# Performance work log

Measured on AMD Instinct MI355X. Metric: run time of the kernel, lower is better.

The kernel has to match this reference:

```python
import jax, jax.numpy as jnp
import numpy as np

B, T, L = 64, 2048, 200
H = KV = 256          # hidden_size == key_value_size (asserted in original)
E = 256               # embed_size
V = 33                # vocab_size
MLP_H = 512
EPS = 1e-12           # F.normalize eps


def _p(k, shape):
    return jax.random.normal(k, shape, dtype=jnp.float32) * 0.05


def setup_inputs() -> dict:
    key = jax.random.key(0)
    ks = jax.random.split(key, 20)
    inp = {
        "key":   jax.random.normal(ks[0], (B, T, KV), dtype=jnp.float32),
        "value": jax.random.normal(ks[1], (B, T, KV), dtype=jnp.float32),
        "labels": jax.random.randint(ks[2], (L, B), 0, V).astype(jnp.int32),
        "final_seq_lens": jax.random.randint(ks[3], (B,), 1, T + 1).astype(jnp.int32),
        # embedding table: vocab_size + 1 rows (SOS/padding extra row)
        "emb": _p(ks[4], (V + 1, E)),
        # LSTMCell 0: input = embed + KV
        "w_ih0": _p(ks[5], (4 * H, E + KV)),
        "w_hh0": _p(ks[6], (4 * H, H)),
        "b_ih0": _p(ks[7], (4 * H,)),
        "b_hh0": _p(ks[8], (4 * H,)),
        # LSTMCells 1..2 (n_layers-1 = 2), stacked
        "w_ih_rest": _p(ks[9], (2, 4 * H, H)),
        "w_hh_rest": _p(ks[10], (2, 4 * H, H)),
        "b_ih_rest": _p(ks[11], (2, 4 * H)),
        "b_hh_rest": _p(ks[12], (2, 4 * H)),
        # MLP head: (H + KV) -> MLP_H -> V
        "fc1_w": _p(ks[13], (MLP_H, H + KV)),
        "fc1_b": _p(ks[14], (MLP_H,)),
        "fc2_w": _p(ks[15], (V, MLP_H)),
        "fc2_b": _p(ks[16], (V,)),
    }
    return inp


def _lstm_cell(x, h, c, w_ih, w_hh, b_ih, b_hh):
    # torch.nn.LSTMCell: gates in order i, f, g, o
    g = x @ w_ih.T + b_ih + h @ w_hh.T + b_hh
    i, f, gg, o = jnp.split(g, 4, axis=-1)
    c2 = jax.nn.sigmoid(f) * c + jax.nn.sigmoid(i) * jnp.tanh(gg)
    h2 = jax.nn.sigmoid(o) * jnp.tanh(c2)
    return h2, c2


def reference(key, value, labels, final_seq_lens, emb,
              w_ih0, w_hh0, b_ih0, b_hh0,
              w_ih_rest, w_hh_rest, b_ih_rest, b_hh_rest,
              fc1_w, fc1_b, fc2_w, fc2_b):
    # key mask over encoder time steps: [B, T]
    mask = (jnp.arange(T)[None, :] < final_seq_lens[:, None]).astype(key.dtype)

    labels_emb = emb[labels]                 # [L, B, E] (teacher forcing inputs)

    h0 = jnp.zeros((3, B, H), dtype=key.dtype)
    c0 = jnp.zeros((3, B, H), dtype=key.dtype)
    ctx0 = jnp.zeros((B, KV), dtype=key.dtype)

    def step(carry, x_t):
        h, c, ctx = carry
        rnn_in = jnp.concatenate([x_t, ctx], axis=-1)        # [B, E+KV]
        nh0, nc0 = _lstm_cell(rnn_in, h[0], c[0], w_ih0, w_hh0, b_ih0, b_hh0)
        hs, cs = [nh0], [nc0]
        prev = nh0
        for li in range(2):
            nhi, nci = _lstm_cell(prev, h[li + 1], c[li + 1],
                                  w_ih_rest[li], w_hh_rest[li],
                                  b_ih_rest[li], b_hh_rest[li])
            hs.append(nhi); cs.append(nci)
            prev = nhi
        rnn_out = prev                                       # [B, H]
        # attention: softmax over T, then mask, then L1 renormalize
        energy = jnp.einsum('btd,bd->bt', key, rnn_out)      # [B, T]
        att = jax.nn.softmax(energy, axis=1) * mask
        att = att / jnp.maximum(att.sum(axis=1, keepdims=True), EPS)
        new_ctx = jnp.einsum('bt,btd->bd', att, value)       # [B, KV]
        z = jnp.concatenate([rnn_out, new_ctx], axis=-1)     # [B, H+KV]
        y_t = jnp.maximum(z @ fc1_w.T + fc1_b, 0.0) @ fc2_w.T + fc2_b  # [B, V]
        return (jnp.stack(hs), jnp.stack(cs), new_ctx), y_t

    _, ys = jax.lax.scan(step, (h0, c0, ctx0), labels_emb)   # ys: [L, B, V]
    y_hat = jnp.transpose(ys, (1, 0, 2))                     # [B, L, V]
    return y_hat
```

## Files before the change

### kernel.cpp

```cpp
#include <hip/hip_runtime.h>
#include <hip/hip_bf16.h>

namespace {
constexpr int B  = 64;
constexpr int T  = 2048;
constexpr int L  = 200;
constexpr int H  = 256;
constexpr int KV = 256;
constexpr int E  = 256;
constexpr int V  = 33;
constexpr int MH = 512;
constexpr int G  = 4 * H;
constexpr int HB = H * B;
constexpr int KVB = KV * B;
constexpr int CS = 50;

constexpr long OFF_H   = 0;
constexpr long OFF_C   = OFF_H  + 2L * 3 * HB;
constexpr long OFF_CTX = OFF_C  + 3L * HB;
constexpr long OFF_Z   = OFF_CTX + 2L * KV * B;
constexpr long OFF_M   = OFF_Z  + 2L * B;
constexpr long OFF_E   = OFF_M  + B;
constexpr long OFF_HID = OFF_E  + (long)B * T;
constexpr long OFF_XE  = OFF_HID + (long)MH * B;
constexpr long FLOATS_OLD = OFF_XE + (long)L * E * B;
constexpr long FLOATBYTES = FLOATS_OLD * 4;
constexpr long KVELEMS = (long)B * T * KV;
constexpr long NEED_BF = FLOATBYTES + 2 * KVELEMS * 2;

constexpr long NOFF      = NEED_BF / 4;
constexpr long NOFF_H01  = NOFF;
constexpr long NOFF_C    = NOFF_H01 + 4L * HB;
constexpr long NOFF_H2   = NOFF_C   + 3L * HB;
constexpr long NOFF_CTXA = NOFF_H2  + (long)(L + 1) * HB;
constexpr long NOFF_ZA   = NOFF_CTXA + (long)(L + 1) * KVB;
constexpr long NOFF_HIDC = NOFF_ZA  + (long)(L + 1) * B;
constexpr long FLOATS_NEW = NOFF_HIDC + (long)CS * MH * B;
constexpr long NEED_NEW   = FLOATS_NEW * 4;
}

__device__ __forceinline__ float sigm(float x) { return 1.f / (1.f + __expf(-x)); }
__device__ __forceinline__ float tanh_f(float x) {
  float xc = fminf(fmaxf(x, -15.f), 15.f);
  float e2 = __expf(2.f * xc);
  return (e2 - 1.f) / (e2 + 1.f);
}
__device__ __forceinline__ ushort f2bf(float x) {
  unsigned u = __float_as_uint(x);
  unsigned r = (u + 0x7fffu + ((u >> 16) & 1u)) >> 16;
  return (ushort)r;
}
__device__ __forceinline__ float bf2f(unsigned v) { return __uint_as_float(v << 16); }

__device__ __forceinline__ float gload(const float* p) {
  return __hip_atomic_load(p, __ATOMIC_RELAXED, __HIP_MEMORY_SCOPE_AGENT);
}
__device__ __forceinline__ void gstore(float* p, float v) {
  __hip_atomic_store(p, v, __ATOMIC_RELAXED, __HIP_MEMORY_SCOPE_AGENT);
}

__device__ __forceinline__ void atomicMaxFloat(float* p, float v) {
  int old = __float_as_int(*p);
  while (__int_as_float(old) < v) {
    int assumed = old;
    old = atomicCAS((int*)p, assumed, __float_as_int(v));
    if (old == assumed) break;
  }
}

__device__ __forceinline__ void gbar(unsigned* bar, unsigned gen) {
  __syncthreads();
  if (threadIdx.x == 0) {
    asm volatile("s_waitcnt vmcnt(0)" ::: "memory");
    const unsigned g = blockIdx.x >> 5;
    unsigned prev = __hip_atomic_fetch_add(bar + g * 64, 1u,
                                           __ATOMIC_RELAXED, __HIP_MEMORY_SCOPE_AGENT);
    if (prev == gen * 32u - 1u)
      __hip_atomic_store(bar + 512 + g * 64, gen,
                         __ATOMIC_RELAXED, __HIP_MEMORY_SCOPE_AGENT);
    unsigned spins = 0;
    if (blockIdx.x == 0) {
      for (;;) {
        unsigned ok = 1;
        #pragma unroll
        for (int i = 0; i < 8; ++i)
          ok &= (__hip_atomic_load(bar + 512 + i * 64,
                                   __ATOMIC_RELAXED, __HIP_MEMORY_SCOPE_AGENT) >= gen);
        if (ok) break;
        __builtin_amdgcn_s_sleep(1);
        if (++spins > 400000u) break;
      }
      #pragma unroll
      for (int i = 0; i < 8; ++i)
        __hip_atomic_store(bar + 1024 + i * 64, gen,
                           __ATOMIC_RELAXED, __HIP_MEMORY_SCOPE_AGENT);
    } else {
      const unsigned* rel = bar + 1024 + g * 64;
      while (__hip_atomic_load(rel, __ATOMIC_RELAXED, __HIP_MEMORY_SCOPE_AGENT) < gen) {
        __builtin_amdgcn_s_sleep(1);
        if (++spins > 400000u) break;
      }
    }
  }
  __syncthreads();
}

__global__ void k_init(float* __restrict__ ws) {
  int i = blockIdx.x * blockDim.x + threadIdx.x;
  if (i < 3 * HB) { ws[OFF_H + i] = 0.f; ws[OFF_C + i] = 0.f; }
  if (i < KV * B) ws[OFF_CTX + i] = 0.f;
  if (i < B)      ws[OFF_Z + i] = 1.f;
}

__global__ void k_init2(float* __restrict__ ws) {
  int i = blockIdx.x * blockDim.x + threadIdx.x;
  if (i < 2048)    ws[OFF_H + i]    = 0.f;
  if (i < 4 * HB)  ws[NOFF_H01 + i] = 0.f;
  if (i < 3 * HB)  ws[NOFF_C + i]   = 0.f;
  if (i < HB)      ws[NOFF_H2 + i]  = 0.f;
  if (i < (long)(L + 1) * KVB) ws[NOFF_CTXA + i] = 0.f;
  if (i < (L + 1) * B) ws[NOFF_ZA + i] = (i < B) ? 1.f : 0.f;
}

__global__ void k_embed(const int* __restrict__ labels, const float* __restrict__ emb,
                        float* __restrict__ xembT) {
  int i = blockIdx.x * blockDim.x + threadIdx.x;
  if (i >= L * E * B) return;
  int b = i & 63, e = (i >> 6) & 255, l = i >> 14;
  int lab = labels[l * B + b];
  xembT[i] = emb[lab * E + e];
}

__global__ void k_cvt(const float4* __restrict__ src, ushort4* __restrict__ dst, int n4) {
  int i = blockIdx.x * blockDim.x + threadIdx.x;
  int stride = gridDim.x * blockDim.x;
  for (int k = i; k < n4; k += stride) {
    float4 v = src[k];
    ushort4 o;
    o.x = f2bf(v.x); o.y = f2bf(v.y); o.z = f2bf(v.z); o.w = f2bf(v.w);
    dst[k] = o;
  }
}

__global__ __launch_bounds__(512, 1) void k_mega(
    const float* __restrict__ wih0, const float* __restrict__ whh0,
    const float* __restrict__ bih0, const float* __restrict__ bhh0,
    const float* __restrict__ wihr, const float* __restrict__ whhr,
    const float* __restrict__ bihr, const float* __restrict__ bhhr,
    const ushort* __restrict__ kbf, const ushort* __restrict__ vbf,
    const int* __restrict__ lens, const float* __restrict__ xe,
    float* __restrict__ h01, float* __restrict__ h2a,
    float* __restrict__ ctxa, float* __restrict__ za,
    unsigned* __restrict__ bar) {
  const int bi  = blockIdx.x;
  const int tid = threadIdx.x;
  const int b   = tid & 63;
  const int q   = (tid >> 6) & 3;
  const int ks  = tid >> 8;

  __shared__ float wA[4][768];
  __shared__ float wB[4][512];
  __shared__ float wC[4][512];
  __shared__ float bs[3][4];
  __shared__ float red[2][4][64];
  __shared__ float4 asum[8][64];
  __shared__ float az[8];

  for (int i = tid; i < 4 * 768; i += 512) {
    int qq = i / 768, o = i - qq * 768;
    wA[qq][o] = (o < 512) ? wih0[(long)(qq * H + bi) * 512 + o]
                          : whh0[(long)(qq * H + bi) * 256 + (o - 512)];
  }
  for (int i = tid; i < 4 * 512; i += 512) {
    int qq = i >> 9, o = i & 511;
    long row = qq * H + bi;
    wB[qq][o] = (o < 256) ? wihr[row * H + o] : whhr[row * H + (o - 256)];
    wC[qq][o] = (o < 256) ? wihr[(long)G * H + row * H + o]
                          : whhr[(long)G * H + row * H + (o - 256)];
  }
  if (tid < 4) {
    bs[0][tid] = bih0[tid * H + bi] + bhh0[tid * H + bi];
    bs[1][tid] = bihr[tid * H + bi] + bhhr[tid * H + bi];
    bs[2][tid] = bihr[G + tid * H + bi] + bhhr[G + tid * H + bi];
  }
  __syncthreads();

  const int ab    = bi >> 2;
  const int aseg  = ((bi & 3) << 3) + (tid >> 6);
  const int alane = tid & 63;
  const int alen  = lens[ab];

  float c0 = 0.f, c1 = 0.f, c2 = 0.f;

  for (int t = 0; t < L; ++t) {
    const int cur = t & 1, nxt = cur ^ 1;
    const float* h0p = h01 + (long)cur * 2 * HB;
    const float* h1p = h0p + HB;
    float* h0n = h01 + (long)nxt * 2 * HB;
    float* h1n = h0n + HB;
    const float* xet  = xe + (long)t * E * B;
    const float* ctxc = ctxa + (long)t * KVB;
    const float* h2p  = h2a + (long)t * HB;
    float* h2n        = h2a + (long)(t + 1) * HB;

    {
      float acc;
      if (ks == 0) {
        float s0 = 0.f, s1 = 0.f, s2 = 0.f, s3 = 0.f;
        const float4* wi4 = (const float4*)wA[q];
        #pragma unroll 4
        for (int k = 0; k < 256; k += 4) {
          float4 w = wi4[k >> 2];
          s0 += w.x * xet[(k)     * B + b];
          s1 += w.y * xet[(k + 1) * B + b];
          s2 += w.z * xet[(k + 2) * B + b];
          s3 += w.w * xet[(k + 3) * B + b];
        }
        float a0 = 0.f, a1 = 0.f;
        const float4* wh4 = (const float4*)(wA[q] + 512);
        #pragma unroll 4
        for (int k = 0; k < 128; k += 4) {
          float4 w = wh4[k >> 2];
          a0 += w.x * gload(&h0p[(k)     * B + b]);
          a1 += w.y * gload(&h0p[(k + 1) * B + b]);
          a0 += w.z * gload(&h0p[(k + 2) * B + b]);
          a1 += w.w * gload(&h0p[(k + 3) * B + b]);
        }
        acc = bs[0][q] + (s0 + s1) + (s2 + s3) + (a0 + a1);
      } else {
        float zz = 1.f / fmaxf(gload(&za[t * B + b]), 1e-12f);
        float s0 = 0.f, s1 = 0.f, s2 = 0.f, s3 = 0.f;
        const float4* wi4 = (const float4*)(wA[q] + 256);
        #pragma unroll 4
        for (int k = 0; k < 256; k += 4) {
          float4 w = wi4[k >> 2];
          s0 += w.x * gload(&ctxc[(k)     * B + b]);
          s1 += w.y * gload(&ctxc[(k + 1) * B + b]);
          s2 += w.z * gload(&ctxc[(k + 2) * B + b]);
          s3 += w.w * gload(&ctxc[(k + 3) * B + b]);
        }
        float a0 = 0.f, a1 = 0.f;
        const float4* wh4 = (const float4*)(wA[q] + 640);
        #pragma unroll 4
        for (int k = 0; k < 128; k += 4) {
          float4 w = wh4[k >> 2];
          a0 += w.x * gload(&h0p[(128 + k) * B + b]);
          a1 += w.y * gload(&h0p[(129 + k) * B + b]);
          a0 += w.z * gload(&h0p[(130 + k) * B + b]);
          a1 += w.w * gload(&h0p[(131 + k) * B + b]);
        }
        acc = ((s0 + s1) + (s2 + s3)) * zz + (a0 + a1);
      }
      red[ks][q][b] = acc;
      __syncthreads();
      if (tid < 64) {
        float gi = red[0][0][tid] + red[1][0][tid];
        float gf = red[0][1][tid] + red[1][1][tid];
        float gg = red[0][2][tid] + red[1][2][tid];
        float go = red[0][3][tid] + red[1][3][tid];
        c0 = sigm(gf) * c0 + sigm(gi) * tanh_f(gg);
        gstore(&h0n[bi * B + tid], sigm(go) * tanh_f(c0));
      }
    }
    gbar(bar, 4 * t + 1);

    {
      const int k0 = ks << 7;
      float a1 = 0.f, a2 = 0.f, a3 = 0.f, a4 = 0.f;
      const float4* wi4 = (const float4*)(wB[q] + k0);
      const float4* wh4 = (const float4*)(wB[q] + 256 + k0);
      #pragma unroll 4
      for (int k = 0; k < 128; k += 4) {
        float4 wi = wi4[k >> 2];
        float4 wh = wh4[k >> 2];
        a1 += wi.x * gload(&h0n[(k0 + k)     * B + b]);
        a2 += wi.y * gload(&h0n[(k0 + k + 1) * B + b]);
        a1 += wi.z * gload(&h0n[(k0 + k + 2) * B + b]);
        a2 += wi.w * gload(&h0n[(k0 + k + 3) * B + b]);
        a3 += wh.x * gload(&h1p[(k0 + k)     * B + b]);
        a4 += wh.y * gload(&h1p[(k0 + k + 1) * B + b]);
        a3 += wh.z * gload(&h1p[(k0 + k + 2) * B + b]);
        a4 += wh.w * gload(&h1p[(k0 + k + 3) * B + b]);
      }
      red[ks][q][b] = (ks ? 0.f : bs[1][q]) + (a1 + a2) + (a3 + a4);
      __syncthreads();
      if (tid < 64) {
        float gi = red[0][0][tid] + red[1][0][tid];
        float gf = red[0][1][tid] + red[1][1][tid];
        float gg = red[0][2][tid] + red[1][2][tid];
        float go = red[0][3][tid] + red[1][3][tid];
        c1 = sigm(gf) * c1 + sigm(gi) * tanh_f(gg);
        gstore(&h1n[bi * B + tid], sigm(go) * tanh_f(c1));
      }
    }
    gbar(bar, 4 * t + 2);

    {
      const int k0 = ks << 7;
      float a1 = 0.f, a2 = 0.f, a3 = 0.f, a4 = 0.f;
      const float4* wi4 = (const float4*)(wC[q] + k0);
      const float4* wh4 = (const float4*)(wC[q] + 256 + k0);
      #pragma unroll 4
      for (int k = 0; k < 128; k += 4) {
        float4 wi = wi4[k >> 2];
        float4 wh = wh4[k >> 2];
        a1 += wi.x * gload(&h1n[(k0 + k)     * B + b]);
        a2 += wi.y * gload(&h1n[(k0 + k + 1) * B + b]);
        a1 += wi.z * gload(&h1n[(k0 + k + 2) * B + b]);
        a2 += wi.w * gload(&h1n[(k0 + k + 3) * B + b]);
        a3 += wh.x * gload(&h2p[(k0 + k)     * B + b]);
        a4 += wh.y * gload(&h2p[(k0 + k + 1) * B + b]);
        a3 += wh.z * gload(&h2p[(k0 + k + 2) * B + b]);
        a4 += wh.w * gload(&h2p[(k0 + k + 3) * B + b]);
      }
      red[ks][q][b] = (ks ? 0.f : bs[2][q]) + (a1 + a2) + (a3 + a4);
      __syncthreads();
      if (tid < 64) {
        float gi = red[0][0][tid] + red[1][0][tid];
        float gf = red[0][1][tid] + red[1][1][tid];
        float gg = red[0][2][tid] + red[1][2][tid];
        float go = red[0][3][tid] + red[1][3][tid];
        c2 = sigm(gf) * c2 + sigm(gi) * tanh_f(gg);
        gstore(&h2n[bi * B + tid], sigm(go) * tanh_f(c2));
      }
    }
    gbar(bar, 4 * t + 3);

    {
      float* ctxn = ctxa + (long)(t + 1) * KVB;
      float q0 = gload(&h2n[(4 * alane + 0) * B + ab]);
      float q1 = gload(&h2n[(4 * alane + 1) * B + ab]);
      float q2 = gload(&h2n[(4 * alane + 2) * B + ab]);
      float q3 = gload(&h2n[(4 * alane + 3) * B + ab]);
      float a0 = 0.f, a1 = 0.f, a2 = 0.f, a3 = 0.f, zp = 0.f;
      for (int r = aseg; r < alen; r += 32) {
        size_t off = ((size_t)(ab * T + r)) * KV + 4 * alane;
        uint2 kd = *(const uint2*)(kbf + off);
        uint2 vd = *(const uint2*)(vbf + off);
        float e = bf2f(kd.x & 0xffffu) * q0
                + __uint_as_float(kd.x & 0xffff0000u) * q1
                + bf2f(kd.y & 0xffffu) * q2
                + __uint_as_float(kd.y & 0xffff0000u) * q3;
        #pragma unroll
        for (int o = 32; o; o >>= 1) e += __shfl_xor(e, o, 64);
        float w = __expf(fminf(e, 50.f));
        a0 += w * bf2f(vd.x & 0xffffu);
        a1 += w * __uint_as_float(vd.x & 0xffff0000u);
        a2 += w * bf2f(vd.y & 0xffffu);
        a3 += w * __uint_as_float(vd.y & 0xffff0000u);
        zp += w;
      }
      int wv = tid >> 6;
      asum[wv][alane] = make_float4(a0, a1, a2, a3);
      if (alane == 0) az[wv] = zp;
      __syncthreads();
      if (tid < 256) {
        const float* as = (const float*)asum;
        float s = as[tid]        + as[256 + tid]  + as[512 + tid]  + as[768 + tid]
                + as[1024 + tid] + as[1280 + tid] + as[1536 + tid] + as[1792 + tid];
        atomicAdd(&ctxn[tid * B + ab], s);
      }
      if (tid == 0) {
        atomicAdd(&za[(t + 1) * B + ab],
                  az[0] + az[1] + az[2] + az[3] + az[4] + az[5] + az[6] + az[7]);
      }
    }
    gbar(bar, 4 * t + 4);
  }
}

__global__ __launch_bounds__(512) void k_cell0(
    const float* __restrict__ wih, const float* __restrict__ whh,
    const float* __restrict__ bih, const float* __restrict__ bhh,
    const float* __restrict__ xe,
    const float* __restrict__ ctx, const float* __restrict__ Z,
    const float* __restrict__ hprev,
    float* __restrict__ hnew, float* __restrict__ cst) {
  int t = threadIdx.x;
  int b = t & 63, q = (t >> 6) & 3, ks = t >> 8;
  int j = blockIdx.x;
  int row = q * H + j;
  float acc = 0.f, s0 = 0.f, s1 = 0.f, s2 = 0.f, s3 = 0.f, a2 = 0.f;
  if (ks == 0) {
    acc = bih[row] + bhh[row];
    const float* wi = wih + (long)row * (E + KV);
    #pragma unroll 4
    for (int k = 0; k < E; k += 4) {
      s0 += wi[k]   * xe[(k)   * B + b];
      s1 += wi[k+1] * xe[(k+1) * B + b];
      s2 += wi[k+2] * xe[(k+2) * B + b];
      s3 += wi[k+3] * xe[(k+3) * B + b];
    }
    const float* wh = whh + (long)row * H;
    #pragma unroll 4
    for (int k = 0; k < 128; k += 2) {
      a2 += wh[k]   * hprev[(k)   * B + b];
      a2 += wh[k+1] * hprev[(k+1) * B + b];
    }
    acc += (s0 + s1) + (s2 + s3) + a2;
  } else {
    float zz = 1.f / fmaxf(Z[b], 1e-12f);
    const float* wi = wih + (long)row * (E + KV) + E;
    #pragma unroll 4
    for (int k = 0; k < KV; k += 4) {
      s0 += wi[k]   * ctx[(k)   * B + b];
      s1 += wi[k+1] * ctx[(k+1) * B + b];
      s2 += wi[k+2] * ctx[(k+2) * B + b];
      s3 += wi[k+3] * ctx[(k+3) * B + b];
    }
    const float* wh = whh + (long)row * H + 128;
    #pragma unroll 4
    for (int k = 0; k < 128; k += 2) {
      a2 += wh[k]   * hprev[(128 + k)     * B + b];
      a2 += wh[k+1] * hprev[(128 + k + 1) * B + b];
    }
    acc = ((s0 + s1) + (s2 + s3)) * zz + a2;
  }
  __shared__ float sh[2][4][64];
  sh[ks][q][b] = acc;
  __syncthreads();
  if (t < 64) {
    int bb = t;
    float gi = sh[0][0][bb] + sh[1][0][bb];
    float gf = sh[0][1][bb] + sh[1][1][bb];
    float gg = sh[0][2][bb] + sh[1][2][bb];
    float go = sh[0][3][bb] + sh[1][3][bb];
    float c = sigm(gf) * cst[j * B + bb] + sigm(gi) * tanh_f(gg);
    float h = sigm(go) * tanh_f(c);
    cst[j * B + bb] = c;
    hnew[j * B + bb] = h;
  }
}

__global__ __launch_bounds__(512) void k_cellr(
    const float* __restrict__ wih, const float* __restrict__ whh,
    const float* __restrict__ bih, const float* __restrict__ bhh,
    const float* __restrict__ hin, const float* __restrict__ hprevL,
    float* __restrict__ hnewL, float* __restrict__ cst,
    float* __restrict__ ctxn, float* __restrict__ Zn, float* __restrict__ m, int aux) {
  int t = threadIdx.x;
  int b = t & 63, q = (t >> 6) & 3, ks = t >> 8;
  int j = blockIdx.x;
  int row = q * H + j;
  if (aux) {
    int gid = blockIdx.x * 512 + t;
    if (gid < KV * B) ctxn[gid] = 0.f;
    if (gid < B) { Zn[gid] = 0.f; m[gid] = -3.4e38f; }
  }
  float acc = ks ? 0.f : (bih[row] + bhh[row]);
  float a1 = 0.f, a2 = 0.f, a3 = 0.f, a4 = 0.f;
  const float* wi = wih + (long)row * H + ks * 128;
  const float* wh = whh + (long)row * H + ks * 128;
  int k0 = ks * 128;
  #pragma unroll 4
  for (int k = 0; k < 128; k += 2) {
    a1 += wi[k]   * hin[(k0 + k)     * B + b];
    a2 += wi[k+1] * hin[(k0 + k + 1) * B + b];
    a3 += wh[k]   * hprevL[(k0 + k)     * B + b];
    a4 += wh[k+1] * hprevL[(k0 + k + 1) * B + b];
  }
  acc += (a1 + a2) + (a3 + a4);
  __shared__ float sh[2][4][64];
  sh[ks][q][b] = acc;
  __syncthreads();
  if (t < 64) {
    int bb = t;
    float gi = sh[0][0][bb] + sh[1][0][bb];
    float gf = sh[0][1][bb] + sh[1][1][bb];
    float gg = sh[0][2][bb] + sh[1][2][bb];
    float go = sh[0][3][bb] + sh[1][3][bb];
    float c = sigm(gf) * cst[j * B + bb] + sigm(gi) * tanh_f(gg);
    float h = sigm(go) * tanh_f(c);
    cst[j * B + bb] = c;
    hnewL[j * B + bb] = h;
  }
}

__global__ __launch_bounds__(256) void k_fc1c(
    const float* __restrict__ w, const float* __restrict__ bias,
    const float* __restrict__ h2a, const float* __restrict__ ctxa,
    const float* __restrict__ za, float* __restrict__ hidc, int t0) {
  int s = blockIdx.y;
  int t = t0 + s;
  const float* h2  = h2a  + (long)(t + 1) * HB;
  const float* ctx = ctxa + (long)(t + 1) * KVB;
  int tid = threadIdx.x;
  int b = tid & 63, jl = tid >> 6;
  int j = blockIdx.x * 4 + jl;
  float zz = 1.f / fmaxf(za[(t + 1) * B + b], 1e-12f);
  const float* wr = w + (long)j * (H + KV);
  float s0 = 0.f, s1 = 0.f, c0 = 0.f, c1 = 0.f;
  #pragma unroll 4
  for (int k = 0; k < 256; k += 2) {
    s0 += wr[k]       * h2[(k)   * B + b];
    s1 += wr[k+1]     * h2[(k+1) * B + b];
    c0 += wr[256 + k]   * ctx[(k)   * B + b];
    c1 += wr[256 + k+1] * ctx[(k+1) * B + b];
  }
  float acc = bias[j] + (s0 + s1) + (c0 + c1) * zz;
  hidc[((long)s * MH + j) * B + b] = fmaxf(acc, 0.f);
}

__global__ __launch_bounds__(64) void k_fc2c(
    const float* __restrict__ w, const float* __restrict__ bias,
    const float* __restrict__ hidc, float* __restrict__ out, int t0) {
  int s = blockIdx.y;
  int v = blockIdx.x;
  int b = threadIdx.x;
  const float* hid = hidc + (long)s * MH * B;
  const float* wr = w + (long)v * MH;
  float s0 = 0.f, s1 = 0.f, s2 = 0.f, s3 = 0.f;
  #pragma unroll 4
  for (int k = 0; k < MH; k += 4) {
    s0 += wr[k]   * hid[(k)   * B + b];
    s1 += wr[k+1] * hid[(k+1) * B + b];
    s2 += wr[k+2] * hid[(k+2) * B + b];
    s3 += wr[k+3] * hid[(k+3) * B + b];
  }
  out[((long)b * L + (t0 + s)) * V + v] = bias[v] + (s0 + s1) + (s2 + s3);
}

template <int BF>
__global__ __launch_bounds__(256) void k_energy(
    const void* __restrict__ keyp, const float* __restrict__ h2,
    const int* __restrict__ lens, float* __restrict__ e, float* __restrict__ m) {
  int b = blockIdx.y;
  int len = lens[b];
  int wave = threadIdx.x >> 6, lane = threadIdx.x & 63;
  int t0 = (blockIdx.x * 4 + wave) * 16;
  if (t0 >= len) return;
  float h0 = h2[(4 * lane + 0) * B + b];
  float h1 = h2[(4 * lane + 1) * B + b];
  float h2v = h2[(4 * lane + 2) * B + b];
  float h3 = h2[(4 * lane + 3) * B + b];
  int tend = min(t0 + 16, len);
  float wmax = -3.4e38f;
  for (int t = t0; t < tend; t++) {
    float4 kv;
    if (BF) {
      const uint2* p = (const uint2*)((const ushort*)keyp + (size_t)(b * T + t) * KV + 4 * lane);
      uint2 d = *p;
      kv.x = bf2f(d.x & 0xffffu);
      kv.y = __uint_as_float(d.x & 0xffff0000u);
      kv.z = bf2f(d.y & 0xffffu);
      kv.w = __uint_as_float(d.y & 0xffff0000u);
    } else {
      kv = ((const float4*)((const float*)keyp + (size_t)(b * T + t) * KV))[lane];
    }
    float s = kv.x * h0 + kv.y * h1 + kv.z * h2v + kv.w * h3;
    #pragma unroll
    for (int off = 32; off; off >>= 1) s += __shfl_xor(s, off, 64);
    if (lane == 0) e[b * T + t] = s;
    wmax = fmaxf(wmax, s);
  }
  if (lane == 0) atomicMaxFloat(&m[b], wmax);
}

template <int BF>
__global__ __launch_bounds__(256) void k_pv(
    const void* __restrict__ valp, const float* __restrict__ e, const float* __restrict__ m,
    const int* __restrict__ lens, float* __restrict__ ctxn, float* __restrict__ Zn) {
  int b = blockIdx.y;
  int len = lens[b];
  int t0blk = blockIdx.x * 256;
  if (t0blk >= len) return;
  int wave = threadIdx.x >> 6, lane = threadIdx.x & 63;
  float mb = m[b];
  float a0 = 0.f, a1 = 0.f, a2 = 0.f, a3 = 0.f, zp = 0.f;
  int t0 = t0blk + wave * 64;
  int tend = min(t0 + 64, len);
  for (int t = t0; t < tend; t++) {
    float w = __expf(e[b * T + t] - mb);
    float4 vv;
    if (BF) {
      const uint2* p = (const uint2*)((const ushort*)valp + (size_t)(b * T + t) * KV + 4 * lane);
      uint2 d = *p;
      vv.x = bf2f(d.x & 0xffffu);
      vv.y = __uint_as_float(d.x & 0xffff0000u);
      vv.z = bf2f(d.y & 0xffffu);
      vv.w = __uint_as_float(d.y & 0xffff0000u);
    } else {
      vv = ((const float4*)((const float*)valp + (size_t)(b * T + t) * KV))[lane];
    }
    a0 += w * vv.x; a1 += w * vv.y; a2 += w * vv.z; a3 += w * vv.w;
    zp += w;
  }
  __shared__ float sh[4][256];
  __shared__ float shz[4];
  sh[wave][4 * lane + 0] = a0;
  sh[wave][4 * lane + 1] = a1;
  sh[wave][4 * lane + 2] = a2;
  sh[wave][4 * lane + 3] = a3;
  if (lane == 0) shz[wave] = zp;
  __syncthreads();
  if (wave == 0) {
    #pragma unroll
    for (int r = 0; r < 4; r++) {
      int d = lane * 4 + r;
      float s = sh[0][d] + sh[1][d] + sh[2][d] + sh[3][d];
      atomicAdd(&ctxn[d * B + b], s);
    }
    if (lane == 0) atomicAdd(&Zn[b], shz[0] + shz[1] + shz[2] + shz[3]);
  }
}

__global__ __launch_bounds__(256) void k_fc1(
    const float* __restrict__ w, const float* __restrict__ bias,
    const float* __restrict__ h2, const float* __restrict__ ctxn, const float* __restrict__ Zn,
    float* __restrict__ hid) {
  int t = threadIdx.x;
  int b = t & 63, jl = t >> 6;
  int j = blockIdx.x * 4 + jl;
  float zz = 1.f / fmaxf(Zn[b], 1e-12f);
  const float* wr = w + (long)j * (H + KV);
  float s0 = 0.f, s1 = 0.f, s2 = 0.f, s3 = 0.f, a2 = 0.f, a3 = 0.f;
  #pragma unroll 4
  for (int k = 0; k < H; k += 4) {
    s0 += wr[k]   * h2[(k)   * B + b];
    s1 += wr[k+1] * h2[(k+1) * B + b];
    s2 += wr[k+2] * h2[(k+2) * B + b];
    s3 += wr[k+3] * h2[(k+3) * B + b];
  }
  #pragma unroll 4
  for (int k = 0; k < KV; k += 2) {
    a2 += wr[H + k]     * ctxn[(k)   * B + b];
    a3 += wr[H + k + 1] * ctxn[(k+1) * B + b];
  }
  float acc = bias[j] + (s0 + s1) + (s2 + s3) + (a2 + a3) * zz;
  hid[j * B + b] = fmaxf(acc, 0.f);
}

__global__ __launch_bounds__(64) void k_fc2(
    const float* __restrict__ w, const float* __restrict__ bias,
    const float* __restrict__ hid, float* __restrict__ out, int step) {
  int b = threadIdx.x;
  int v = blockIdx.x;
  const float* wr = w + (long)v * MH;
  float s0 = 0.f, s1 = 0.f, s2 = 0.f, s3 = 0.f;
  #pragma unroll 4
  for (int k = 0; k < MH; k += 4) {
    s0 += wr[k]   * hid[(k)   * B + b];
    s1 += wr[k+1] * hid[(k+1) * B + b];
    s2 += wr[k+2] * hid[(k+2) * B + b];
    s3 += wr[k+3] * hid[(k+3) * B + b];
  }
  out[((long)b * L + step) * V + v] = bias[v] + (s0 + s1) + (s2 + s3);
}

static void launch_legacy(const float* key, const float* value, const int* lens,
                          const float* w_ih0, const float* w_hh0,
                          const float* b_ih0, const float* b_hh0,
                          const float* w_ihr, const float* w_hhr,
                          const float* b_ihr, const float* b_hhr,
                          const float* fc1_w, const float* fc1_b,
                          const float* fc2_w, const float* fc2_b,
                          float* out, float* ws,
                          const ushort* kbf, const ushort* vbf, bool bf,
                          hipStream_t stream) {
  float* hbuf = ws + OFF_H;
  float* cbuf = ws + OFF_C;
  float* ctxb = ws + OFF_CTX;
  float* Zb   = ws + OFF_Z;
  float* mb   = ws + OFF_M;
  float* eb   = ws + OFF_E;
  float* hid  = ws + OFF_HID;
  float* xe   = ws + OFF_XE;
  for (int t = 0; t < L; t++) {
    int cur = t & 1, nxt = cur ^ 1;
    float* hprev = hbuf + (long)cur * 3 * HB;
    float* hnew  = hbuf + (long)nxt * 3 * HB;
    float* ctxc  = ctxb + (long)cur * KV * B;
    float* ctxn  = ctxb + (long)nxt * KV * B;
    float* Zc = Zb + cur * B;
    float* Zn = Zb + nxt * B;

    k_cell0<<<H, 512, 0, stream>>>(w_ih0, w_hh0, b_ih0, b_hh0,
                                   xe + (long)t * E * B, ctxc, Zc,
                                   hprev, hnew, cbuf);
    k_cellr<<<H, 512, 0, stream>>>(w_ihr, w_hhr, b_ihr, b_hhr,
                                   hnew, hprev + HB, hnew + HB, cbuf + HB,
                                   ctxn, Zn, mb, 1);
    k_cellr<<<H, 512, 0, stream>>>(w_ihr + (long)G * H, w_hhr + (long)G * H,
                                   b_ihr + G, b_hhr + G,
                                   hnew + HB, hprev + 2 * HB, hnew + 2 * HB, cbuf + 2 * HB,
                                   nullptr, nullptr, nullptr, 0);
    if (bf) {
      k_energy<1><<<dim3(T / 64, B), 256, 0, stream>>>(kbf, hnew + 2 * HB, lens, eb, mb);
      k_pv<1><<<dim3(T / 256, B), 256, 0, stream>>>(vbf, eb, mb, lens, ctxn, Zn);
    } else {
      k_energy<0><<<dim3(T / 64, B), 256, 0, stream>>>(key, hnew + 2 * HB, lens, eb, mb);
      k_pv<0><<<dim3(T / 256, B), 256, 0, stream>>>(value, eb, mb, lens, ctxn, Zn);
    }
    k_fc1<<<MH / 4, 256, 0, stream>>>(fc1_w, fc1_b, hnew + 2 * HB, ctxn, Zn, hid);
    k_fc2<<<V, 64, 0, stream>>>(fc2_w, fc2_b, hid, out, t);
  }
}

extern "C" void kernel_launch(void* const* d_in, const int* in_sizes, int n_in,
                              void* d_out, int out_size, void* d_ws, size_t ws_size,
                              hipStream_t stream) {
  const float* key    = (const float*)d_in[0];
  const float* value  = (const float*)d_in[1];
  const int*   labels = (const int*)d_in[2];
  const int*   lens   = (const int*)d_in[3];
  const float* emb    = (const float*)d_in[4];
  const float* w_ih0  = (const float*)d_in[5];
  const float* w_hh0  = (const float*)d_in[6];
  const float* b_ih0  = (const float*)d_in[7];
  const float* b_hh0  = (const float*)d_in[8];
  const float* w_ihr  = (const float*)d_in[9];
  const float* w_hhr  = (const float*)d_in[10];
  const float* b_ihr  = (const float*)d_in[11];
  const float* b_hhr  = (const float*)d_in[12];
  const float* fc1_w  = (const float*)d_in[13];
  const float* fc1_b  = (const float*)d_in[14];
  const float* fc2_w  = (const float*)d_in[15];
  const float* fc2_b  = (const float*)d_in[16];
  float* out = (float*)d_out;
  float* ws  = (float*)d_ws;

  bool bf      = ((long)ws_size >= NEED_BF);
  bool newpath = ((long)ws_size >= NEED_NEW);
  ushort* kbf = (ushort*)((char*)d_ws + FLOATBYTES);
  ushort* vbf = kbf + KVELEMS;

  k_embed<<<(L * E * B + 255) / 256, 256, 0, stream>>>(labels, emb, ws + OFF_XE);
  if (bf) {
    int n4 = (int)(KVELEMS >> 2);
    k_cvt<<<4096, 256, 0, stream>>>((const float4*)key, (ushort4*)kbf, n4);
    k_cvt<<<4096, 256, 0, stream>>>((const float4*)value, (ushort4*)vbf, n4);
  }

  if (newpath) {
    k_init2<<<(int)(((long)(L + 1) * KVB + 255) / 256), 256, 0, stream>>>(ws);
    float* h01  = ws + NOFF_H01;
    float* h2a  = ws + NOFF_H2;
    float* ctxa = ws + NOFF_CTXA;
    float* za   = ws + NOFF_ZA;
    float* hidc = ws + NOFF_HIDC;
    float* xep  = ws + OFF_XE;
    unsigned* bar = (unsigned*)(ws + OFF_H);

    k_mega<<<256, 512, 0, stream>>>(w_ih0, w_hh0, b_ih0, b_hh0,
                                    w_ihr, w_hhr, b_ihr, b_hhr,
                                    kbf, vbf, lens, xep,
                                    h01, h2a, ctxa, za, bar);

    for (int c = 0; c < L / CS; c++) {
      int t0 = c * CS;
      k_fc1c<<<dim3(MH / 4, CS), 256, 0, stream>>>(fc1_w, fc1_b, h2a, ctxa, za, hidc, t0);
      k_fc2c<<<dim3(V, CS), 64, 0, stream>>>(fc2_w, fc2_b, hidc, out, t0);
    }
  } else {
    k_init<<<(3 * HB + 255) / 256, 256, 0, stream>>>(ws);
    launch_legacy(key, value, lens, w_ih0, w_hh0, b_ih0, b_hh0,
                  w_ihr, w_hhr, b_ihr, b_hhr, fc1_w, fc1_b, fc2_w, fc2_b,
                  out, ws, kbf, vbf, bf, stream);
  }
}
```

Before: 14.48 ms.

## Stage recurrent state vectors into LDS with wide coherent loads before dot products

Each LSTM layer phase now first copies the full 256x64 state or context vector from global memory into a 64KB shared buffer using eight coherent dwordx4 loads per thread, then runs the matvec from LDS. Before, each thread issued many scalar atomic-relaxed global loads. The layer-0 work split is also rebalanced: both halves of the block share the recurrent-weight dot product, while the input terms stay split between embedding and context. The aim is to replace many uncoalesced scalar coherent loads with a few wide ones, at the cost of extra __syncthreads, 64KB more LDS, and serialized staging.

```diff
diff --git a/kernel.cpp b/kernel.cpp
--- a/kernel.cpp
+++ b/kernel.cpp
@@ -66,6 +66,38 @@
     old = atomicCAS((int*)p, assumed, __float_as_int(v));
     if (old == assumed) break;
   }
+}
+
+__device__ __forceinline__ void stage64(const float* __restrict__ g,
+                                        float* __restrict__ lds, int tid) {
+  const float4* s = (const float4*)g;
+  const float4* p0 = s + tid;
+  const float4* p1 = s + tid + 512;
+  const float4* p2 = s + tid + 1024;
+  const float4* p3 = s + tid + 1536;
+  const float4* p4 = s + tid + 2048;
+  const float4* p5 = s + tid + 2560;
+  const float4* p6 = s + tid + 3072;
+  const float4* p7 = s + tid + 3584;
+  float4 r0, r1, r2, r3, r4, r5, r6, r7;
+  asm volatile("global_load_dwordx4 %0, %1, off sc0 sc1" : "=v"(r0) : "v"(p0));
+  asm volatile("global_load_dwordx4 %0, %1, off sc0 sc1" : "=v"(r1) : "v"(p1));
+  asm volatile("global_load_dwordx4 %0, %1, off sc0 sc1" : "=v"(r2) : "v"(p2));
+  asm volatile("global_load_dwordx4 %0, %1, off sc0 sc1" : "=v"(r3) : "v"(p3));
+  asm volatile("global_load_dwordx4 %0, %1, off sc0 sc1" : "=v"(r4) : "v"(p4));
+  asm volatile("global_load_dwordx4 %0, %1, off sc0 sc1" : "=v"(r5) : "v"(p5));
+  asm volatile("global_load_dwordx4 %0, %1, off sc0 sc1" : "=v"(r6) : "v"(p6));
+  asm volatile("global_load_dwordx4 %0, %1, off sc0 sc1" : "=v"(r7) : "v"(p7));
+  asm volatile("s_waitcnt vmcnt(0)" ::: "memory");
+  float4* d = (float4*)lds;
+  d[tid]        = r0;
+  d[tid + 512]  = r1;
+  d[tid + 1024] = r2;
+  d[tid + 1536] = r3;
+  d[tid + 2048] = r4;
+  d[tid + 2560] = r5;
+  d[tid + 3072] = r6;
+  d[tid + 3584] = r7;
 }
 
 __device__ __forceinline__ void gbar(unsigned* bar, unsigned gen) {
@@ -113,13 +145,13 @@
 }
 
 __global__ void k_init2(float* __restrict__ ws) {
-  int i = blockIdx.x * blockDim.x + threadIdx.x;
-  if (i < 2048)    ws[OFF_H + i]    = 0.f;
-  if (i < 4 * HB)  ws[NOFF_H01 + i] = 0.f;
-  if (i < 3 * HB)  ws[NOFF_C + i]   = 0.f;
-  if (i < HB)      ws[NOFF_H2 + i]  = 0.f;
-  if (i < (long)(L + 1) * KVB) ws[NOFF_CTXA + i] = 0.f;
-  if (i < (L + 1) * B) ws[NOFF_ZA + i] = (i < B) ? 1.f : 0.f;
+  long i = (long)blockIdx.x * blockDim.x + threadIdx.x;
+  if (i < 2048)    gstore(&ws[OFF_H + i], 0.f);
+  if (i < 4 * HB)  gstore(&ws[NOFF_H01 + i], 0.f);
+  if (i < 3 * HB)  gstore(&ws[NOFF_C + i], 0.f);
+  if (i < HB)      gstore(&ws[NOFF_H2 + i], 0.f);
+  if (i < (long)(L + 1) * KVB) gstore(&ws[NOFF_CTXA + i], 0.f);
+  if (i < (L + 1) * B) gstore(&ws[NOFF_ZA + i], (i < B) ? 1.f : 0.f);
 }
 
 __global__ void k_embed(const int* __restrict__ labels, const float* __restrict__ emb,
@@ -165,6 +197,7 @@
   __shared__ float red[2][4][64];
   __shared__ float4 asum[8][64];
   __shared__ float az[8];
+  __shared__ float st[16384];
 
   for (int i = tid; i < 4 * 768; i += 512) {
     int qq = i / 768, o = i - qq * 768;
@@ -204,7 +237,9 @@
     float* h2n        = h2a + (long)(t + 1) * HB;
 
     {
-      float acc;
+      stage64(ctxc, st, tid);
+      __syncthreads();
+      float sdot;
       if (ks == 0) {
         float s0 = 0.f, s1 = 0.f, s2 = 0.f, s3 = 0.f;
         const float4* wi4 = (const float4*)wA[q];
@@ -216,42 +251,38 @@
           s2 += w.z * xet[(k + 2) * B + b];
           s3 += w.w * xet[(k + 3) * B + b];
         }
-        float a0 = 0.f, a1 = 0.f;
-        const float4* wh4 = (const float4*)(wA[q] + 512);
-        #pragma unroll 4
-        for (int k = 0; k < 128; k += 4) {
-          float4 w = wh4[k >> 2];
-          a0 += w.x * gload(&h0p[(k)     * B + b]);
-          a1 += w.y * gload(&h0p[(k + 1) * B + b]);
-          a0 += w.z * gload(&h0p[(k + 2) * B + b]);
-          a1 += w.w * gload(&h0p[(k + 3) * B + b]);
-        }
-        acc = bs[0][q] + (s0 + s1) + (s2 + s3) + (a0 + a1);
+        sdot = (s0 + s1) + (s2 + s3);
       } else {
         float zz = 1.f / fmaxf(gload(&za[t * B + b]), 1e-12f);
         float s0 = 0.f, s1 = 0.f, s2 = 0.f, s3 = 0.f;
         const float4* wi4 = (const float4*)(wA[q] + 256);
-        #pragma unroll 4
+        #pragma unroll 8
         for (int k = 0; k < 256; k += 4) {
           float4 w = wi4[k >> 2];
-          s0 += w.x * gload(&ctxc[(k)     * B + b]);
-          s1 += w.y * gload(&ctxc[(k + 1) * B + b]);
-          s2 += w.z * gload(&ctxc[(k + 2) * B + b]);
-          s3 += w.w * gload(&ctxc[(k + 3) * B + b]);
+          s0 += w.x * st[(k)     * 64 + b];
+          s1 += w.y * st[(k + 1) * 64 + b];
+          s2 += w.z * st[(k + 2) * 64 + b];
+          s3 += w.w * st[(k + 3) * 64 + b];
         }
+        sdot = ((s0 + s1) + (s2 + s3)) * zz;
+      }
+      __syncthreads();
+      stage64(h0p, st, tid);
+      __syncthreads();
+      {
+        const int kh = ks << 7;
         float a0 = 0.f, a1 = 0.f;
-        const float4* wh4 = (const float4*)(wA[q] + 640);
-        #pragma unroll 4
+        const float4* wh4 = (const float4*)(wA[q] + 512 + kh);
+        #pragma unroll 8
         for (int k = 0; k < 128; k += 4) {
           float4 w = wh4[k >> 2];
-          a0 += w.x * gload(&h0p[(128 + k) * B + b]);
-          a1 += w.y * gload(&h0p[(129 + k) * B + b]);
-          a0 += w.z * gload(&h0p[(130 + k) * B + b]);
-          a1 += w.w * gload(&h0p[(131 + k) * B + b]);
+          a0 += w.x * st[(kh + k)     * 64 + b];
+          a1 += w.y * st[(kh + k + 1) * 64 + b];
+          a0 += w.z * st[(kh + k + 2) * 64 + b];
+          a1 += w.w * st[(kh + k + 3) * 64 + b];
         }
-        acc = ((s0 + s1) + (s2 + s3)) * zz + (a0 + a1);
-      }
-      red[ks][q][b] = acc;
+        red[ks][q][b] = (ks ? 0.f : bs[0][q]) + sdot + (a0 + a1);
+      }
       __syncthreads();
       if (tid < 64) {
         float gi = red[0][0][tid] + red[1][0][tid];
@@ -265,24 +296,36 @@
     gbar(bar, 4 * t + 1);
 
     {
+      stage64(h0n, st, tid);
+      __syncthreads();
       const int k0 = ks << 7;
-      float a1 = 0.f, a2 = 0.f, a3 = 0.f, a4 = 0.f;
-      const float4* wi4 = (const float4*)(wB[q] + k0);
-      const float4* wh4 = (const float4*)(wB[q] + 256 + k0);
-      #pragma unroll 4
-      for (int k = 0; k < 128; k += 4) {
-        float4 wi = wi4[k >> 2];
-        float4 wh = wh4[k >> 2];
-        a1 += wi.x * gload(&h0n[(k0 + k)     * B + b]);
-        a2 += wi.y * gload(&h0n[(k0 + k + 1) * B + b]);
-        a1 += wi.z * gload(&h0n[(k0 + k + 2) * B + b]);
-        a2 += wi.w * gload(&h0n[(k0 + k + 3) * B + b]);
-        a3 += wh.x * gload(&h1p[(k0 + k)     * B + b]);
-        a4 += wh.y * gload(&h1p[(k0 + k + 1) * B + b]);
-        a3 += wh.z * gload(&h1p[(k0 + k + 2) * B + b]);
-        a4 += wh.w * gload(&h1p[(k0 + k + 3) * B + b]);
-      }
-      red[ks][q][b] = (ks ? 0.f : bs[1][q]) + (a1 + a2) + (a3 + a4);
+      float a1 = 0.f, a2 = 0.f;
+      {
+        const float4* wi4 = (const float4*)(wB[q] + k0);
+        #pragma unroll 8
+        for (int k = 0; k < 128; k += 4) {
+          float4 wi = wi4[k >> 2];
+          a1 += wi.x * st[(k0 + k)     * 64 + b];
+          a2 += wi.y * st[(k0 + k + 1) * 64 + b];
+          a1 += wi.z * st[(k0 + k + 2) * 64 + b];
+          a2 += wi.w * st[(k0 + k + 3) * 64 + b];
+        }
+      }
+      __syncthreads();
+      stage64(h1p, st, tid);
+      __syncthreads();
+      {
+        const float4* wh4 = (const float4*)(wB[q] + 256 + k0);
+        #pragma unroll 8
+        for (int k = 0; k < 128; k += 4) {
+          float4 wh = wh4[k >> 2];
+          a1 += wh.x * st[(k0 + k)     * 64 + b];
+          a2 += wh.y * st[(k0 + k + 1) * 64 + b];
+          a1 += wh.z * st[(k0 + k + 2) * 64 + b];
+          a2 += wh.w * st[(k0 + k + 3) * 64 + b];
+        }
+      }
+      red[ks][q][b] = (ks ? 0.f : bs[1][q]) + (a1 + a2);
       __syncthreads();
       if (tid < 64) {
         float gi = red[0][0][tid] + red[1][0][tid];
@@ -296,24 +339,36 @@
     gbar(bar, 4 * t + 2);
 
     {
+      stage64(h1n, st, tid);
+      __syncthreads();
       const int k0 = ks << 7;
-      float a1 = 0.f, a2 = 0.f, a3 = 0.f, a4 = 0.f;
-      const float4* wi4 = (const float4*)(wC[q] + k0);
-      const float4* wh4 = (const float4*)(wC[q] + 256 + k0);
-      #pragma unroll 4
-      for (int k = 0; k < 128; k += 4) {
-        float4 wi = wi4[k >> 2];
-        float4 wh = wh4[k >> 2];
-        a1 += wi.x * gload(&h1n[(k0 + k)     * B + b]);
-        a2 += wi.y * gload(&h1n[(k0 + k + 1) * B + b]);
-        a1 += wi.z * gload(&h1n[(k0 + k + 2) * B + b]);
-        a2 += wi.w * gload(&h1n[(k0 + k + 3) * B + b]);
-        a3 += wh.x * gload(&h2p[(k0 + k)     * B + b]);
-        a4 += wh.y * gload(&h2p[(k0 + k + 1) * B + b]);
-        a3 += wh.z * gload(&h2p[(k0 + k + 2) * B + b]);
-        a4 += wh.w * gload(&h2p[(k0 + k + 3) * B + b]);
-      }
-      red[ks][q][b] = (ks ? 0.f : bs[2][q]) + (a1 + a2) + (a3 + a4);
+      float a1 = 0.f, a2 = 0.f;
+      {
+        const float4* wi4 = (const float4*)(wC[q] + k0);
+        #pragma unroll 8
+        for (int k = 0; k < 128; k += 4) {
+          float4 wi = wi4[k >> 2];
+          a1 += wi.x * st[(k0 + k)     * 64 + b];
+          a2 += wi.y * st[(k0 + k + 1) * 64 + b];
+          a1 += wi.z * st[(k0 + k + 2) * 64 + b];
+          a2 += wi.w * st[(k0 + k + 3) * 64 + b];
+        }
+      }
+      __syncthreads();
+      stage64(h2p, st, tid);
+      __syncthreads();
+      {
+        const float4* wh4 = (const float4*)(wC[q] + 256 + k0);
+        #pragma unroll 8
+        for (int k = 0; k < 128; k += 4) {
+          float4 wh = wh4[k >> 2];
+          a1 += wh.x * st[(k0 + k)     * 64 + b];
+          a2 += wh.y * st[(k0 + k + 1) * 64 + b];
+          a1 += wh.z * st[(k0 + k + 2) * 64 + b];
+          a2 += wh.w * st[(k0 + k + 3) * 64 + b];
+        }
+      }
+      red[ks][q][b] = (ks ? 0.f : bs[2][q]) + (a1 + a2);
       __syncthreads();
       if (tid < 64) {
         float gi = red[0][0][tid] + red[1][0][tid];
```

After: 14.40 ms. About the same (-0.5%).
